# Optimization experiments

Hardware: AMD Instinct MI355X
Metric: run time of the kernel (lower is better)

The kernel has to match this reference:

```python
import jax, jax.numpy as jnp
import numpy as np

TAU = 0.5
EPS = 1e-8  # torch CosineSimilarity eps


def _normalize(v):
    # matches torch cosine sim: divide by max(||v||, eps)
    n = jnp.linalg.norm(v, axis=-1, keepdims=True)
    return v / jnp.maximum(n, EPS)


def setup_inputs() -> dict:
    key = jax.random.key(0)
    k1, k2 = jax.random.split(key)
    N, D = 4096, 256
    x = jax.random.normal(k1, (N, D), dtype=jnp.float32)
    y = jax.random.normal(k2, (N, D), dtype=jnp.float32)
    return {"x": x, "y": y}


def reference(x, y):
    n = x.shape[0]
    xn = _normalize(x)
    yn = _normalize(y)
    inv_tau = 1.0 / TAU
    sim_xx = (xn @ xn.T) * inv_tau  # [n, n]
    sim_yy = (yn @ yn.T) * inv_tau
    sim_xy = (xn @ yn.T) * inv_tau
    neg_inf = jnp.float32(-jnp.inf)
    diag = jnp.arange(n)
    sim_xx = sim_xx.at[diag, diag].set(neg_inf)
    sim_yy = sim_yy.at[diag, diag].set(neg_inf)
    scores1 = jnp.concatenate([sim_xy, sim_xx], axis=-1)          # [n, 2n]
    scores2 = jnp.concatenate([sim_yy, sim_xy.T], axis=-1)        # [n, 2n]
    scores = jnp.concatenate([scores1, scores2], axis=-2)          # [2n, 2n]
    targets = jnp.arange(2 * n)
    logp = jax.nn.log_softmax(scores, axis=-1)
    loss = -jnp.mean(logp[jnp.arange(2 * n), targets])
    return loss
```

## Files before the change

### kernel.cpp

```cpp
#include <hip/hip_runtime.h>
#include <hip/hip_bf16.h>


#define NROWS 8192
#define DDIM  256
#define BM    128
#define BN    64
#define COLSPLIT 8
#define COLS_PER (NROWS / COLSPLIT)
#define NT (COLS_PER / BN)

typedef __attribute__((ext_vector_type(8))) __bf16 bf16x8_t;
typedef __attribute__((ext_vector_type(4))) float  f32x4_t;

typedef __attribute__((address_space(1))) const void* as1_cvp;
typedef __attribute__((address_space(3))) void*       as3_vp;

#if __has_builtin(__builtin_amdgcn_exp2f)
#define EXP2F __builtin_amdgcn_exp2f
#else
#define EXP2F exp2f
#endif

#define TWO_LOG2E 2.8853900817779268f

__global__ __launch_bounds__(256) void normalize_diag_kernel(
    const float* __restrict__ x, const float* __restrict__ y,
    __hip_bfloat16* __restrict__ zb, float* __restrict__ rowdiag,
    float* __restrict__ rowsum) {
  const int g = blockIdx.x * 256 + threadIdx.x;
  if (g < NROWS) rowsum[g] = 0.f;

  const int w = threadIdx.x >> 6, lane = threadIdx.x & 63;
  const int i = blockIdx.x * 4 + w;
  const float4 xv = ((const float4*)(x + (size_t)i * DDIM))[lane];
  const float4 yv = ((const float4*)(y + (size_t)i * DDIM))[lane];
  float ssx = xv.x * xv.x + xv.y * xv.y + xv.z * xv.z + xv.w * xv.w;
  float ssy = yv.x * yv.x + yv.y * yv.y + yv.z * yv.z + yv.w * yv.w;
  float sxy = xv.x * yv.x + xv.y * yv.y + xv.z * yv.z + xv.w * yv.w;
  #pragma unroll
  for (int off = 32; off > 0; off >>= 1) {
    ssx += __shfl_xor(ssx, off, 64);
    ssy += __shfl_xor(ssy, off, 64);
    sxy += __shfl_xor(sxy, off, 64);
  }
  const float sclx = 1.0f / fmaxf(sqrtf(ssx), 1e-8f);
  const float scly = 1.0f / fmaxf(sqrtf(ssy), 1e-8f);
  __hip_bfloat16 px[4], py[4];
  px[0] = __float2bfloat16(xv.x * sclx); px[1] = __float2bfloat16(xv.y * sclx);
  px[2] = __float2bfloat16(xv.z * sclx); px[3] = __float2bfloat16(xv.w * sclx);
  py[0] = __float2bfloat16(yv.x * scly); py[1] = __float2bfloat16(yv.y * scly);
  py[2] = __float2bfloat16(yv.z * scly); py[3] = __float2bfloat16(yv.w * scly);
  *(short4*)(zb + (size_t)i * DDIM + lane * 4)            = *(short4*)px;
  *(short4*)(zb + (size_t)(i + 4096) * DDIM + lane * 4)   = *(short4*)py;
  if (lane == 0) rowdiag[i] = 2.0f * sxy * sclx * scly;
}

__global__ __launch_bounds__(256) void gram_lse_kernel(
    const __hip_bfloat16* __restrict__ zbh, float* __restrict__ rowsum) {
  __shared__ short smem[2][BN * DDIM];

  const short* zs = (const short*)zbh;
  const char* zbytes = (const char*)zs;
  const int tid  = threadIdx.x;
  const int w    = tid >> 6;
  const int lane = tid & 63;
  const int lhi  = lane >> 4;
  const int llo  = lane & 15;
  const int i0 = (blockIdx.x >> 3) * BM;
  const int c0 = (blockIdx.x & 7) * COLS_PER;
  const bool has_diag = ((blockIdx.x >> 6) == (blockIdx.x & 7));

  const int arow0 = i0 + w * 32 + llo;
  const float TBF = __bfloat162float(__float2bfloat16(TWO_LOG2E));
  bf16x8_t afa[8], afb[8];
  #pragma unroll
  for (int ks = 0; ks < 8; ++ks) {
    afa[ks] = *(const bf16x8_t*)(zs + (size_t)arow0 * DDIM + ks * 32 + lhi * 8);
    afb[ks] = *(const bf16x8_t*)(zs + (size_t)(arow0 + 16) * DDIM + ks * 32 + lhi * 8);
    #pragma unroll
    for (int e = 0; e < 8; ++e) {
      afa[ks][e] = (__bf16)((float)afa[ks][e] * TBF);
      afb[ks][e] = (__bf16)((float)afb[ks][e] * TBF);
    }
  }

  int soff[8], loff[8];
  #pragma unroll
  for (int it = 0; it < 8; ++it) {
    const int o    = it * 4096 + tid * 16;
    const int cr   = o >> 9;
    const int slot = (o >> 4) & 31;
    soff[it] = cr * 512 + ((slot ^ (cr & 31)) << 4);
    loff[it] = it * 4096 + w * 1024;
  }

#define STAGE(buf, ct_) do {                                                  \
    const size_t cbase = (size_t)(c0 + (ct_) * BN) * 512;                     \
    _Pragma("unroll")                                                         \
    for (int it = 0; it < 8; ++it) {                                          \
      __builtin_amdgcn_global_load_lds(                                       \
          (as1_cvp)(zbytes + cbase + (size_t)soff[it]),                       \
          (as3_vp)((char*)smem[buf] + loff[it]), 16, 0, 0);                   \
    }                                                                         \
  } while (0)

  float racc0[4] = {0.f, 0.f, 0.f, 0.f};
  float racc1[4] = {0.f, 0.f, 0.f, 0.f};
  const int gr0 = i0 + w * 32 + lhi * 4;
  const int gr1 = gr0 + 16;

  STAGE(0, 0);
  asm volatile("s_waitcnt vmcnt(0)" ::: "memory");
  __syncthreads();
  int cur = 0;

  for (int ct = 0; ct < NT; ++ct) {
    if (ct + 1 < NT) STAGE(cur ^ 1, ct + 1);
    const int cb = c0 + ct * BN;

    #pragma unroll
    for (int nt = 0; nt < 4; ++nt) {
      const int cr = nt * 16 + llo;
      f32x4_t acc0 = {0.f, 0.f, 0.f, 0.f};
      f32x4_t acc1 = {0.f, 0.f, 0.f, 0.f};
      #pragma unroll
      for (int ks = 0; ks < 8; ++ks) {
        const int kg = ks * 4 + lhi;
        const bf16x8_t bfrag = *(const bf16x8_t*)(
            (const char*)smem[cur] + cr * 512 + ((kg ^ (cr & 31)) << 4));
        acc0 = __builtin_amdgcn_mfma_f32_16x16x32_bf16(afa[ks], bfrag, acc0, 0, 0, 0);
        acc1 = __builtin_amdgcn_mfma_f32_16x16x32_bf16(afb[ks], bfrag, acc1, 0, 0, 0);
      }
      if (has_diag) {
        const int gc = cb + cr;
        #pragma unroll
        for (int j = 0; j < 4; ++j) {
          racc0[j] += ((gr0 + j) != gc) ? EXP2F(acc0[j]) : 0.f;
          racc1[j] += ((gr1 + j) != gc) ? EXP2F(acc1[j]) : 0.f;
        }
      } else {
        #pragma unroll
        for (int j = 0; j < 4; ++j) {
          racc0[j] += EXP2F(acc0[j]);
          racc1[j] += EXP2F(acc1[j]);
        }
      }
    }
    asm volatile("s_waitcnt vmcnt(0)" ::: "memory");
    __syncthreads();
    cur ^= 1;
  }
#undef STAGE

  #pragma unroll
  for (int j = 0; j < 4; ++j) {
    float v0 = racc0[j], v1 = racc1[j];
    v0 += __shfl_xor(v0, 1, 16); v1 += __shfl_xor(v1, 1, 16);
    v0 += __shfl_xor(v0, 2, 16); v1 += __shfl_xor(v1, 2, 16);
    v0 += __shfl_xor(v0, 4, 16); v1 += __shfl_xor(v1, 4, 16);
    v0 += __shfl_xor(v0, 8, 16); v1 += __shfl_xor(v1, 8, 16);
    if (llo == 0) {
      atomicAdd(&rowsum[gr0 + j], v0);
      atomicAdd(&rowsum[gr1 + j], v1);
    }
  }
}

__global__ __launch_bounds__(256) void finalize_kernel(
    const float* __restrict__ rowsum, const float* __restrict__ rowdiag,
    float* __restrict__ out) {
  const int t = threadIdx.x;
  float s = 0.f;
  for (int r4 = t; r4 < NROWS / 4; r4 += 256) {
    const float4 v = ((const float4*)rowsum)[r4];
    s += __logf(v.x) + __logf(v.y) + __logf(v.z) + __logf(v.w);
  }
  for (int i4 = t; i4 < 4096 / 4; i4 += 256) {
    const float4 d = ((const float4*)rowdiag)[i4];
    s -= 2.0f * (d.x + d.y + d.z + d.w);
  }
  #pragma unroll
  for (int off = 32; off > 0; off >>= 1) s += __shfl_xor(s, off, 64);
  __shared__ float wsum[4];
  const int w = t >> 6, lane = t & 63;
  if (lane == 0) wsum[w] = s;
  __syncthreads();
  if (t == 0) out[0] = (wsum[0] + wsum[1] + wsum[2] + wsum[3]) / (float)NROWS;
}

extern "C" void kernel_launch(void* const* d_in, const int* in_sizes, int n_in,
                              void* d_out, int out_size, void* d_ws, size_t ws_size,
                              hipStream_t stream) {
  const float* x = (const float*)d_in[0];
  const float* y = (const float*)d_in[1];
  float* out = (float*)d_out;

  char* ws = (char*)d_ws;
  __hip_bfloat16* zb = (__hip_bfloat16*)ws;
  float* rowsum  = (float*)(ws + (size_t)NROWS * DDIM * 2);
  float* rowdiag = rowsum + NROWS;

  normalize_diag_kernel<<<1024, 256, 0, stream>>>(x, y, zb, rowdiag, rowsum);
  gram_lse_kernel<<<512, 256, 0, stream>>>(zb, rowsum);
  finalize_kernel<<<1, 256, 0, stream>>>(rowsum, rowdiag, out);
}
```

Baseline: 55.16 us.

## Double the row tile per block and fuse finalize into the last block

The Gram/LSE kernel now runs 512 threads per block, covering 256 rows against 512 columns, instead of 256 threads covering 128 rows against 1024 columns. Each staged B tile is therefore reused by twice as many A rows, which cuts LDS fill traffic per output. The separate finalize launch is removed: blocks increment a global counter after a threadfence, and the last block reads rowsum atomically and writes the loss. This saves a kernel launch and its gap, but leaves a serial tail in one block and raises per-block register and LDS pressure.

Result: slower. 114.7 us (+108.0%).

```diff
diff --git a/kernel.cpp b/kernel.cpp
--- a/kernel.cpp
+++ b/kernel.cpp
@@ -4,11 +4,12 @@
 
 #define NROWS 8192
 #define DDIM  256
-#define BM    128
+#define BM    256
 #define BN    64
-#define COLSPLIT 8
+#define COLSPLIT 16
 #define COLS_PER (NROWS / COLSPLIT)
 #define NT (COLS_PER / BN)
+#define NBLOCKS 512
 
 typedef __attribute__((ext_vector_type(8))) __bf16 bf16x8_t;
 typedef __attribute__((ext_vector_type(4))) float  f32x4_t;
@@ -27,9 +28,10 @@
 __global__ __launch_bounds__(256) void normalize_diag_kernel(
     const float* __restrict__ x, const float* __restrict__ y,
     __hip_bfloat16* __restrict__ zb, float* __restrict__ rowdiag,
-    float* __restrict__ rowsum) {
+    float* __restrict__ rowsum, int* __restrict__ counter) {
   const int g = blockIdx.x * 256 + threadIdx.x;
   if (g < NROWS) rowsum[g] = 0.f;
+  if (g == 0) *counter = 0;
 
   const int w = threadIdx.x >> 6, lane = threadIdx.x & 63;
   const int i = blockIdx.x * 4 + w;
@@ -56,8 +58,10 @@
   if (lane == 0) rowdiag[i] = 2.0f * sxy * sclx * scly;
 }
 
-__global__ __launch_bounds__(256) void gram_lse_kernel(
-    const __hip_bfloat16* __restrict__ zbh, float* __restrict__ rowsum) {
+__global__ __launch_bounds__(512) void gram_lse_kernel(
+    const __hip_bfloat16* __restrict__ zbh, float* __restrict__ rowsum,
+    const float* __restrict__ rowdiag, int* __restrict__ counter,
+    float* __restrict__ out) {
   __shared__ short smem[2][BN * DDIM];
 
   const short* zs = (const short*)zbh;
@@ -67,9 +71,9 @@
   const int lane = tid & 63;
   const int lhi  = lane >> 4;
   const int llo  = lane & 15;
-  const int i0 = (blockIdx.x >> 3) * BM;
-  const int c0 = (blockIdx.x & 7) * COLS_PER;
-  const bool has_diag = ((blockIdx.x >> 6) == (blockIdx.x & 7));
+  const int i0 = (blockIdx.x >> 4) * BM;
+  const int c0 = (blockIdx.x & 15) * COLS_PER;
+  const bool has_diag = ((blockIdx.x >> 5) == (blockIdx.x & 15));
 
   const int arow0 = i0 + w * 32 + llo;
   const float TBF = __bfloat162float(__float2bfloat16(TWO_LOG2E));
@@ -85,20 +89,20 @@
     }
   }
 
-  int soff[8], loff[8];
-  #pragma unroll
-  for (int it = 0; it < 8; ++it) {
-    const int o    = it * 4096 + tid * 16;
+  int soff[4], loff[4];
+  #pragma unroll
+  for (int it = 0; it < 4; ++it) {
+    const int o    = it * 8192 + tid * 16;
     const int cr   = o >> 9;
     const int slot = (o >> 4) & 31;
     soff[it] = cr * 512 + ((slot ^ (cr & 31)) << 4);
-    loff[it] = it * 4096 + w * 1024;
+    loff[it] = it * 8192 + w * 1024;
   }
 
 #define STAGE(buf, ct_) do {                                                  \
     const size_t cbase = (size_t)(c0 + (ct_) * BN) * 512;                     \
     _Pragma("unroll")                                                         \
-    for (int it = 0; it < 8; ++it) {                                          \
+    for (int it = 0; it < 4; ++it) {                                          \
       __builtin_amdgcn_global_load_lds(                                       \
           (as1_cvp)(zbytes + cbase + (size_t)soff[it]),                       \
           (as3_vp)((char*)smem[buf] + loff[it]), 16, 0, 0);                   \
@@ -165,28 +169,30 @@
       atomicAdd(&rowsum[gr1 + j], v1);
     }
   }
-}
-
-__global__ __launch_bounds__(256) void finalize_kernel(
-    const float* __restrict__ rowsum, const float* __restrict__ rowdiag,
-    float* __restrict__ out) {
-  const int t = threadIdx.x;
+
+  __threadfence();
+  __shared__ int lastflag;
+  if (tid == 0) lastflag = (atomicAdd(counter, 1) == NBLOCKS - 1);
+  __syncthreads();
+  if (!lastflag) return;
+
   float s = 0.f;
-  for (int r4 = t; r4 < NROWS / 4; r4 += 256) {
-    const float4 v = ((const float4*)rowsum)[r4];
-    s += __logf(v.x) + __logf(v.y) + __logf(v.z) + __logf(v.w);
-  }
-  for (int i4 = t; i4 < 4096 / 4; i4 += 256) {
-    const float4 d = ((const float4*)rowdiag)[i4];
-    s -= 2.0f * (d.x + d.y + d.z + d.w);
-  }
+  for (int r = tid; r < NROWS; r += 512) {
+    const float v = atomicAdd(&rowsum[r], 0.0f);
+    s += __logf(v);
+  }
+  for (int i = tid; i < 4096; i += 512) s -= 2.0f * rowdiag[i];
   #pragma unroll
   for (int off = 32; off > 0; off >>= 1) s += __shfl_xor(s, off, 64);
-  __shared__ float wsum[4];
-  const int w = t >> 6, lane = t & 63;
-  if (lane == 0) wsum[w] = s;
+  __shared__ float wsum2[8];
+  if (lane == 0) wsum2[w] = s;
   __syncthreads();
-  if (t == 0) out[0] = (wsum[0] + wsum[1] + wsum[2] + wsum[3]) / (float)NROWS;
+  if (tid == 0) {
+    float t = 0.f;
+    #pragma unroll
+    for (int k = 0; k < 8; ++k) t += wsum2[k];
+    out[0] = t / (float)NROWS;
+  }
 }
 
 extern "C" void kernel_launch(void* const* d_in, const int* in_sizes, int n_in,
@@ -200,8 +206,8 @@
   __hip_bfloat16* zb = (__hip_bfloat16*)ws;
   float* rowsum  = (float*)(ws + (size_t)NROWS * DDIM * 2);
   float* rowdiag = rowsum + NROWS;
-
-  normalize_diag_kernel<<<1024, 256, 0, stream>>>(x, y, zb, rowdiag, rowsum);
-  gram_lse_kernel<<<512, 256, 0, stream>>>(zb, rowsum);
-  finalize_kernel<<<1, 256, 0, stream>>>(rowsum, rowdiag, out);
+  int*   counter = (int*)(rowdiag + 4096);
+
+  normalize_diag_kernel<<<1024, 256, 0, stream>>>(x, y, zb, rowdiag, rowsum, counter);
+  gram_lse_kernel<<<NBLOCKS, 512, 0, stream>>>(zb, rowsum, rowdiag, counter, out);
 }
```
